# Optimization experiments

Hardware: AMD Instinct MI355X
Metric: run time of the kernel (lower is better)

The kernel has to match this reference:

```python
import jax, jax.numpy as jnp
import numpy as np

N_NODES = 262144
N_EDGES = 1048576
N_GRAPHS = 8192
IN_CH, HID, OUT_CH, N_LAYERS = 64, 256, 1, 3
SLOPE = 0.1  # LeakyReLU negative slope


def setup_inputs() -> dict:
    key = jax.random.key(0)
    ks = jax.random.split(key, 12)
    s = 0.05  # weight scale for numerical sanity
    return {
        "x": jax.random.normal(ks[0], (N_NODES, IN_CH), jnp.float32),
        "edge_index": jax.random.randint(ks[1], (2, N_EDGES), 0, N_NODES, jnp.int64),
        "batch": jnp.sort(jax.random.randint(ks[2], (N_NODES,), 0, N_GRAPHS, jnp.int64)),
        "embed_w": jax.random.normal(ks[3], (IN_CH, HID), jnp.float32) * s,
        "embed_b": jax.random.normal(ks[4], (HID,), jnp.float32) * s,
        "lin_l_w": jax.random.normal(ks[5], (N_LAYERS, HID, HID), jnp.float32) * s,
        "lin_l_b": jax.random.normal(ks[6], (N_LAYERS, HID), jnp.float32) * s,
        "lin_r_w": jax.random.normal(ks[7], (N_LAYERS, HID, HID), jnp.float32) * s,
        "lin1_w": jax.random.normal(ks[8], (HID, HID), jnp.float32) * s,
        "lin1_b": jax.random.normal(ks[9], (HID,), jnp.float32) * s,
        "lin2_w": jax.random.normal(ks[10], (HID, OUT_CH), jnp.float32) * s,
        "lin2_b": jax.random.normal(ks[11], (OUT_CH,), jnp.float32) * s,
    }


def reference(x, edge_index, batch, embed_w, embed_b, lin_l_w, lin_l_b, lin_r_w,
              lin1_w, lin1_b, lin2_w, lin2_b):
    n = x.shape[0]
    src, dst = edge_index[0], edge_index[1]  # messages flow src -> dst (PyG)
    # in-degree for mean aggregation, clamped to avoid div-by-zero
    deg = jax.ops.segment_sum(jnp.ones((src.shape[0],), x.dtype), dst, num_segments=n)
    inv_deg = (1.0 / jnp.maximum(deg, 1.0))[:, None]  # [N,1]

    h = x @ embed_w + embed_b  # [N, HID]
    for i in range(N_LAYERS):
        agg = jax.ops.segment_sum(h[src], dst, num_segments=n) * inv_deg  # mean over neighbors
        h = agg @ lin_l_w[i] + lin_l_b[i] + h @ lin_r_w[i]  # SAGEConv: lin_l(mean) + lin_r(x)
        if i < N_LAYERS - 1:
            h = jax.nn.leaky_relu(h, SLOPE)
    # global_add_pool over graphs in the batch
    pooled = jax.ops.segment_sum(h, batch, num_segments=N_GRAPHS)  # [G, HID]
    h = jax.nn.leaky_relu(pooled @ lin1_w + lin1_b, SLOPE)
    return h @ lin2_w + lin2_b  # [G, OUT_CH]
```

## Files before the change

kernel.cpp:

```cpp
#include <hip/hip_runtime.h>

typedef unsigned short u16;
typedef __bf16 bf16x8 __attribute__((ext_vector_type(8)));
typedef float f32x4 __attribute__((ext_vector_type(4)));
typedef unsigned short us8v __attribute__((ext_vector_type(8)));
typedef unsigned short us4v __attribute__((ext_vector_type(4)));

constexpr int NN = 262144;
constexpr int NE = 1048576;
constexpr int NG = 8192;
#define SLOPEF 0.1f

__device__ __forceinline__ float lrelu(float v) { return v > 0.f ? v : SLOPEF * v; }

__device__ __forceinline__ u16 f2bf(float f) {
  unsigned u = __builtin_bit_cast(unsigned, f);
  u += 0x7FFFu + ((u >> 16) & 1u);
  return (u16)(u >> 16);
}
__device__ __forceinline__ float bf2f(u16 s) {
  return __builtin_bit_cast(float, ((unsigned)s) << 16);
}

__device__ __align__(256) u16   g_HB[(size_t)NN * 256];
__device__ __align__(256) u16   g_AGG[(size_t)NN * 256];
__device__ __align__(256) u16   g_WTe[256 * 64];
__device__ __align__(256) u16   g_WTl[3 * 256 * 512];
__device__ __align__(256) int   g_indptr[NN + 1];
__device__ __align__(256) int   g_cursor[NN];
__device__ __align__(256) int   g_colsrc[NE];
__device__ __align__(256) int   g_bsum[256];
__device__ __align__(256) int   g_boff[256];
__device__ __align__(256) int   g_degi[NN];
__device__ __align__(256) float g_pooled[(size_t)NG * 256];

__global__ __launch_bounds__(256) void k_zero_deg() {
  g_degi[blockIdx.x * 256 + threadIdx.x] = 0;
}
__global__ __launch_bounds__(256) void k_zero_pool() {
  ((float4*)g_pooled)[blockIdx.x * 256 + threadIdx.x] = make_float4(0.f, 0.f, 0.f, 0.f);
}

__global__ __launch_bounds__(256) void k_convw(const float* __restrict__ embed_w,
    const float* __restrict__ lin_l_w, const float* __restrict__ lin_r_w) {
  int t = blockIdx.x * 256 + threadIdx.x;
  if (t < 16384) {
    int n = t >> 6, k = t & 63;
    g_WTe[t] = f2bf(embed_w[k * 256 + n]);
  } else {
    int u = t - 16384;
    int l = u >> 17;
    int r = u & 131071;
    int n = r >> 9, k = r & 511;
    float v = (k < 256) ? lin_l_w[(size_t)l * 65536 + k * 256 + n]
                        : lin_r_w[(size_t)l * 65536 + (k - 256) * 256 + n];
    g_WTl[(size_t)l * 131072 + n * 512 + k] = f2bf(v);
  }
}

__global__ __launch_bounds__(256) void k_deg(const int* __restrict__ dst) {
  int e = blockIdx.x * 256 + threadIdx.x;
  atomicAdd(&g_degi[dst[e]], 1);
}

__global__ __launch_bounds__(256) void k_scan1() {
  __shared__ int sm[256];
  int b = blockIdx.x, t = threadIdx.x;
  int4 v = *(const int4*)(g_degi + (size_t)b * 1024 + t * 4);
  int s = v.x + v.y + v.z + v.w;
  sm[t] = s; __syncthreads();
  for (int off = 1; off < 256; off <<= 1) {
    int x = (t >= off) ? sm[t - off] : 0; __syncthreads();
    sm[t] += x; __syncthreads();
  }
  if (t == 255) g_bsum[b] = sm[255];
}

__global__ __launch_bounds__(256) void k_scan2() {
  __shared__ int sm[256];
  int t = threadIdx.x;
  int v = g_bsum[t];
  sm[t] = v; __syncthreads();
  for (int off = 1; off < 256; off <<= 1) {
    int x = (t >= off) ? sm[t - off] : 0; __syncthreads();
    sm[t] += x; __syncthreads();
  }
  g_boff[t] = sm[t] - v;
  if (t == 255) g_indptr[NN] = sm[255];
}

__global__ __launch_bounds__(256) void k_scan3() {
  __shared__ int sm[256];
  int b = blockIdx.x, t = threadIdx.x;
  int4 v = *(const int4*)(g_degi + (size_t)b * 1024 + t * 4);
  int s = v.x + v.y + v.z + v.w;
  sm[t] = s; __syncthreads();
  for (int off = 1; off < 256; off <<= 1) {
    int x = (t >= off) ? sm[t - off] : 0; __syncthreads();
    sm[t] += x; __syncthreads();
  }
  int base = g_boff[b] + sm[t] - s;
  int i0 = b * 1024 + t * 4;
  g_indptr[i0]     = base;
  g_indptr[i0 + 1] = base + v.x;
  g_indptr[i0 + 2] = base + v.x + v.y;
  g_indptr[i0 + 3] = base + v.x + v.y + v.z;
}

__global__ __launch_bounds__(256) void k_invcur() {
  int n = blockIdx.x * 256 + threadIdx.x;
  float inv = 1.0f / fmaxf((float)g_degi[n], 1.0f);
  ((float*)g_degi)[n] = inv;
  g_cursor[n] = g_indptr[n];
}

__global__ __launch_bounds__(256) void k_fill(const int* __restrict__ ei) {
  int e = blockIdx.x * 256 + threadIdx.x;
  int src = ei[e], dst = ei[NE + e];
  int p = atomicAdd(&g_cursor[dst], 1);
  g_colsrc[p] = src;
}

__global__ __launch_bounds__(256) void k_gather() {
  int n = blockIdx.x * 4 + (threadIdx.x >> 6);
  int lane = threadIdx.x & 63;
  int s = g_indptr[n], e = g_indptr[n + 1];
  float a0 = 0.f, a1 = 0.f, a2 = 0.f, a3 = 0.f;
  for (int i = s; i < e; ++i) {
    int src = g_colsrc[i];
    us4v v = *(const us4v*)(g_HB + (size_t)src * 256 + lane * 4);
    a0 += bf2f(v[0]); a1 += bf2f(v[1]); a2 += bf2f(v[2]); a3 += bf2f(v[3]);
  }
  float w = ((const float*)g_degi)[n];
  us4v o;
  o[0] = f2bf(a0 * w); o[1] = f2bf(a1 * w); o[2] = f2bf(a2 * w); o[3] = f2bf(a3 * w);
  *(us4v*)(g_AGG + (size_t)n * 256 + lane * 4) = o;
}

template<int KSTEPS, int AMODE, bool LEAKY>
__global__ __launch_bounds__(256) void k_gemm(
    const float* __restrict__ Axf, const float* __restrict__ bias, int layer) {
  __shared__ __align__(16) unsigned char As[8192];
  __shared__ __align__(16) unsigned char Bs[32768];
  constexpr int LDW = AMODE ? 512 : 64;
  const u16* __restrict__ WT = AMODE ? (g_WTl + (size_t)layer * 131072) : g_WTe;
  const int tid = threadIdx.x;
  const int lane = tid & 63;
  const int w = tid >> 6;
  const int wr = w >> 1, wc = w & 1;
  const int m0 = blockIdx.x * 64;
  const int tg = tid & 7, tr = tid >> 3;

  f32x4 acc[2][8];
#pragma unroll
  for (int mi = 0; mi < 2; ++mi)
#pragma unroll
    for (int nj = 0; nj < 8; ++nj) acc[mi][nj] = (f32x4){0.f, 0.f, 0.f, 0.f};

  for (int s = 0; s < KSTEPS; ++s) {
    const int k0 = s * 64;
    us8v areg0, areg1;
    if (AMODE == 0) {
      const float* p0 = Axf + (size_t)(m0 + tr) * 64 + tg * 8;
      const float* p1 = Axf + (size_t)(m0 + tr + 32) * 64 + tg * 8;
      float4 f0 = *(const float4*)p0, f1 = *(const float4*)(p0 + 4);
      float4 g0 = *(const float4*)p1, g1 = *(const float4*)(p1 + 4);
      areg0[0] = f2bf(f0.x); areg0[1] = f2bf(f0.y); areg0[2] = f2bf(f0.z); areg0[3] = f2bf(f0.w);
      areg0[4] = f2bf(f1.x); areg0[5] = f2bf(f1.y); areg0[6] = f2bf(f1.z); areg0[7] = f2bf(f1.w);
      areg1[0] = f2bf(g0.x); areg1[1] = f2bf(g0.y); areg1[2] = f2bf(g0.z); areg1[3] = f2bf(g0.w);
      areg1[4] = f2bf(g1.x); areg1[5] = f2bf(g1.y); areg1[6] = f2bf(g1.z); areg1[7] = f2bf(g1.w);
    } else {
      const u16* src = (k0 < 256) ? (g_AGG + k0) : (g_HB + (k0 - 256));
      areg0 = *(const us8v*)(src + (size_t)(m0 + tr) * 256 + tg * 8);
      areg1 = *(const us8v*)(src + (size_t)(m0 + tr + 32) * 256 + tg * 8);
    }
    us8v breg[8];
#pragma unroll
    for (int it = 0; it < 8; ++it)
      breg[it] = *(const us8v*)(WT + (size_t)(tr + 32 * it) * LDW + k0 + tg * 8);
    __syncthreads();
    *(us8v*)(As + tg * 1024 + tr * 16) = areg0;
    *(us8v*)(As + tg * 1024 + (tr + 32) * 16) = areg1;
#pragma unroll
    for (int it = 0; it < 8; ++it)
      *(us8v*)(Bs + tg * 4096 + (tr + 32 * it) * 16) = breg[it];
    __syncthreads();
#pragma unroll
    for (int ks = 0; ks < 2; ++ks) {
      const int gsel = ks * 4 + (lane >> 4);
      bf16x8 a0 = *(const bf16x8*)(As + gsel * 1024 + (wr * 32 + (lane & 15)) * 16);
      bf16x8 a1 = *(const bf16x8*)(As + gsel * 1024 + (wr * 32 + 16 + (lane & 15)) * 16);
#pragma unroll
      for (int nj = 0; nj < 8; ++nj) {
        bf16x8 b = *(const bf16x8*)(Bs + gsel * 4096 + (wc * 128 + nj * 16 + (lane & 15)) * 16);
        acc[0][nj] = __builtin_amdgcn_mfma_f32_16x16x32_bf16(a0, b, acc[0][nj], 0, 0, 0);
        acc[1][nj] = __builtin_amdgcn_mfma_f32_16x16x32_bf16(a1, b, acc[1][nj], 0, 0, 0);
      }
    }
  }
#pragma unroll
  for (int mi = 0; mi < 2; ++mi)
#pragma unroll
    for (int nj = 0; nj < 8; ++nj) {
      const int col = wc * 128 + nj * 16 + (lane & 15);
      const float bb = bias[col];
#pragma unroll
      for (int j = 0; j < 4; ++j) {
        const int row = m0 + wr * 32 + mi * 16 + (lane >> 4) * 4 + j;
        float v = acc[mi][nj][j] + bb;
        if (LEAKY) v = lrelu(v);
        g_HB[(size_t)row * 256 + col] = f2bf(v);
      }
    }
}

__global__ __launch_bounds__(256) void k_pool(const int* __restrict__ batch) {
  int c = threadIdx.x;
  int n0 = blockIdx.x * 64;
  int gprev = batch[n0];
  float acc = 0.f;
  for (int i = 0; i < 64; ++i) {
    int n = n0 + i;
    int g = batch[n];
    if (g != gprev) {
      unsafeAtomicAdd(&g_pooled[(size_t)gprev * 256 + c], acc);
      acc = 0.f; gprev = g;
    }
    acc += bf2f(g_HB[(size_t)n * 256 + c]);
  }
  unsafeAtomicAdd(&g_pooled[(size_t)gprev * 256 + c], acc);
}

__global__ __launch_bounds__(256) void k_head(const float* __restrict__ w1,
    const float* __restrict__ b1, const float* __restrict__ w2, const float* __restrict__ b2,
    float* __restrict__ out) {
  __shared__ float p[256];
  __shared__ float red[256];
  int g = blockIdx.x, c = threadIdx.x;
  p[c] = g_pooled[(size_t)g * 256 + c];
  __syncthreads();
  float acc = b1[c];
#pragma unroll 8
  for (int k = 0; k < 256; ++k) acc = fmaf(p[k], w1[k * 256 + c], acc);
  acc = lrelu(acc) * w2[c];
  red[c] = acc;
  __syncthreads();
  for (int s = 128; s > 0; s >>= 1) {
    if (c < s) red[c] += red[c + s];
    __syncthreads();
  }
  if (c == 0) out[g] = red[0] + b2[0];
}

extern "C" void kernel_launch(void* const* d_in, const int* in_sizes, int n_in,
                              void* d_out, int out_size, void* d_ws, size_t ws_size,
                              hipStream_t stream) {
  const float* x       = (const float*)d_in[0];
  const int*   ei      = (const int*)d_in[1];
  const int*   batch   = (const int*)d_in[2];
  const float* embed_w = (const float*)d_in[3];
  const float* embed_b = (const float*)d_in[4];
  const float* lin_l_w = (const float*)d_in[5];
  const float* lin_l_b = (const float*)d_in[6];
  const float* lin_r_w = (const float*)d_in[7];
  const float* lin1_w  = (const float*)d_in[8];
  const float* lin1_b  = (const float*)d_in[9];
  const float* lin2_w  = (const float*)d_in[10];
  const float* lin2_b  = (const float*)d_in[11];
  float* out = (float*)d_out;
  (void)d_ws; (void)ws_size; (void)in_sizes; (void)n_in; (void)out_size;

  k_zero_deg <<<NN / 256, 256, 0, stream>>>();
  k_zero_pool<<<NG * 256 / (4 * 256), 256, 0, stream>>>();
  k_convw<<<(16384 + 3 * 131072) / 256, 256, 0, stream>>>(embed_w, lin_l_w, lin_r_w);
  k_deg  <<<NE / 256, 256, 0, stream>>>(ei + NE);
  k_scan1<<<256, 256, 0, stream>>>();
  k_scan2<<<1, 256, 0, stream>>>();
  k_scan3<<<256, 256, 0, stream>>>();
  k_invcur<<<NN / 256, 256, 0, stream>>>();
  k_fill <<<NE / 256, 256, 0, stream>>>(ei);

  k_gemm<1, 0, false><<<NN / 64, 256, 0, stream>>>(x, embed_b, 0);

  for (int i = 0; i < 3; ++i) {
    k_gather<<<NN / 4, 256, 0, stream>>>();
    const float* bb = lin_l_b + (size_t)i * 256;
    if (i < 2)
      k_gemm<8, 1, true><<<NN / 64, 256, 0, stream>>>(nullptr, bb, i);
    else
      k_gemm<8, 1, false><<<NN / 64, 256, 0, stream>>>(nullptr, bb, i);
  }

  k_pool<<<NN / 64, 256, 0, stream>>>(batch);
  k_head<<<NG, 256, 0, stream>>>(lin1_w, lin1_b, lin2_w, lin2_b, out);
}
```

Baseline: 1.444 ms.

## Enlarge GEMM row tile to 128 with swizzled LDS layout and unroll gather

The GEMM kernel now processes 128 rows per block instead of 64. Each wave computes a 64x128 output tile, which doubles reuse of the weight tile loaded into shared memory and halves the number of times weights are fetched from global memory. The shared memory layout changes to row-major with an XOR swizzle, meant to avoid bank conflicts on the fragment loads. The neighbor gather loop is unrolled by four so several source-row loads are in flight at once. The cost is more accumulator registers per thread and larger LDS use, which may lower occupancy.

```diff
diff --git a/kernel.cpp b/kernel.cpp
--- a/kernel.cpp
+++ b/kernel.cpp
@@ -126,7 +126,19 @@
   int lane = threadIdx.x & 63;
   int s = g_indptr[n], e = g_indptr[n + 1];
   float a0 = 0.f, a1 = 0.f, a2 = 0.f, a3 = 0.f;
-  for (int i = s; i < e; ++i) {
+  int i = s;
+  for (; i + 4 <= e; i += 4) {
+    int s0 = g_colsrc[i], s1 = g_colsrc[i + 1], s2 = g_colsrc[i + 2], s3 = g_colsrc[i + 3];
+    us4v v0 = *(const us4v*)(g_HB + (size_t)s0 * 256 + lane * 4);
+    us4v v1 = *(const us4v*)(g_HB + (size_t)s1 * 256 + lane * 4);
+    us4v v2 = *(const us4v*)(g_HB + (size_t)s2 * 256 + lane * 4);
+    us4v v3 = *(const us4v*)(g_HB + (size_t)s3 * 256 + lane * 4);
+    a0 += bf2f(v0[0]) + bf2f(v1[0]) + bf2f(v2[0]) + bf2f(v3[0]);
+    a1 += bf2f(v0[1]) + bf2f(v1[1]) + bf2f(v2[1]) + bf2f(v3[1]);
+    a2 += bf2f(v0[2]) + bf2f(v1[2]) + bf2f(v2[2]) + bf2f(v3[2]);
+    a3 += bf2f(v0[3]) + bf2f(v1[3]) + bf2f(v2[3]) + bf2f(v3[3]);
+  }
+  for (; i < e; ++i) {
     int src = g_colsrc[i];
     us4v v = *(const us4v*)(g_HB + (size_t)src * 256 + lane * 4);
     a0 += bf2f(v[0]); a1 += bf2f(v[1]); a2 += bf2f(v[2]); a3 += bf2f(v[3]);
@@ -140,7 +152,7 @@
 template<int KSTEPS, int AMODE, bool LEAKY>
 __global__ __launch_bounds__(256) void k_gemm(
     const float* __restrict__ Axf, const float* __restrict__ bias, int layer) {
-  __shared__ __align__(16) unsigned char As[8192];
+  __shared__ __align__(16) unsigned char As[16384];
   __shared__ __align__(16) unsigned char Bs[32768];
   constexpr int LDW = AMODE ? 512 : 64;
   const u16* __restrict__ WT = AMODE ? (g_WTl + (size_t)layer * 131072) : g_WTe;
@@ -148,65 +160,85 @@
   const int lane = tid & 63;
   const int w = tid >> 6;
   const int wr = w >> 1, wc = w & 1;
-  const int m0 = blockIdx.x * 64;
-  const int tg = tid & 7, tr = tid >> 3;
-
-  f32x4 acc[2][8];
-#pragma unroll
-  for (int mi = 0; mi < 2; ++mi)
+  const int m0 = blockIdx.x * 128;
+  const int srow = tid >> 1;
+  const int sj   = tid & 1;
+
+  f32x4 acc[4][8];
+#pragma unroll
+  for (int mi = 0; mi < 4; ++mi)
 #pragma unroll
     for (int nj = 0; nj < 8; ++nj) acc[mi][nj] = (f32x4){0.f, 0.f, 0.f, 0.f};
 
   for (int s = 0; s < KSTEPS; ++s) {
     const int k0 = s * 64;
-    us8v areg0, areg1;
+    us8v areg[4], breg[8];
     if (AMODE == 0) {
-      const float* p0 = Axf + (size_t)(m0 + tr) * 64 + tg * 8;
-      const float* p1 = Axf + (size_t)(m0 + tr + 32) * 64 + tg * 8;
-      float4 f0 = *(const float4*)p0, f1 = *(const float4*)(p0 + 4);
-      float4 g0 = *(const float4*)p1, g1 = *(const float4*)(p1 + 4);
-      areg0[0] = f2bf(f0.x); areg0[1] = f2bf(f0.y); areg0[2] = f2bf(f0.z); areg0[3] = f2bf(f0.w);
-      areg0[4] = f2bf(f1.x); areg0[5] = f2bf(f1.y); areg0[6] = f2bf(f1.z); areg0[7] = f2bf(f1.w);
-      areg1[0] = f2bf(g0.x); areg1[1] = f2bf(g0.y); areg1[2] = f2bf(g0.z); areg1[3] = f2bf(g0.w);
-      areg1[4] = f2bf(g1.x); areg1[5] = f2bf(g1.y); areg1[6] = f2bf(g1.z); areg1[7] = f2bf(g1.w);
+      const float* p = Axf + (size_t)(m0 + srow) * 64 + sj * 32;
+#pragma unroll
+      for (int i = 0; i < 4; ++i) {
+        float4 f0 = *(const float4*)(p + i * 8);
+        float4 f1 = *(const float4*)(p + i * 8 + 4);
+        areg[i][0] = f2bf(f0.x); areg[i][1] = f2bf(f0.y);
+        areg[i][2] = f2bf(f0.z); areg[i][3] = f2bf(f0.w);
+        areg[i][4] = f2bf(f1.x); areg[i][5] = f2bf(f1.y);
+        areg[i][6] = f2bf(f1.z); areg[i][7] = f2bf(f1.w);
+      }
     } else {
-      const u16* src = (k0 < 256) ? (g_AGG + k0) : (g_HB + (k0 - 256));
-      areg0 = *(const us8v*)(src + (size_t)(m0 + tr) * 256 + tg * 8);
-      areg1 = *(const us8v*)(src + (size_t)(m0 + tr + 32) * 256 + tg * 8);
-    }
-    us8v breg[8];
-#pragma unroll
-    for (int it = 0; it < 8; ++it)
-      breg[it] = *(const us8v*)(WT + (size_t)(tr + 32 * it) * LDW + k0 + tg * 8);
+      const u16* srcb = ((k0 < 256) ? (g_AGG + k0) : (g_HB + (k0 - 256)))
+                        + (size_t)(m0 + srow) * 256 + sj * 32;
+#pragma unroll
+      for (int i = 0; i < 4; ++i) areg[i] = *(const us8v*)(srcb + i * 8);
+    }
+#pragma unroll
+    for (int it = 0; it < 2; ++it) {
+      const int n = srow + it * 128;
+      const u16* srcb = WT + (size_t)n * LDW + k0 + sj * 32;
+#pragma unroll
+      for (int i = 0; i < 4; ++i) breg[it * 4 + i] = *(const us8v*)(srcb + i * 8);
+    }
     __syncthreads();
-    *(us8v*)(As + tg * 1024 + tr * 16) = areg0;
-    *(us8v*)(As + tg * 1024 + (tr + 32) * 16) = areg1;
-#pragma unroll
-    for (int it = 0; it < 8; ++it)
-      *(us8v*)(Bs + tg * 4096 + (tr + 32 * it) * 16) = breg[it];
+#pragma unroll
+    for (int i = 0; i < 4; ++i) {
+      const int g = sj * 4 + i;
+      *(us8v*)(As + srow * 128 + ((g ^ (srow & 7)) << 4)) = areg[i];
+    }
+#pragma unroll
+    for (int it = 0; it < 2; ++it) {
+      const int n = srow + it * 128;
+#pragma unroll
+      for (int i = 0; i < 4; ++i) {
+        const int g = sj * 4 + i;
+        *(us8v*)(Bs + n * 128 + ((g ^ (n & 7)) << 4)) = breg[it * 4 + i];
+      }
+    }
     __syncthreads();
 #pragma unroll
     for (int ks = 0; ks < 2; ++ks) {
       const int gsel = ks * 4 + (lane >> 4);
-      bf16x8 a0 = *(const bf16x8*)(As + gsel * 1024 + (wr * 32 + (lane & 15)) * 16);
-      bf16x8 a1 = *(const bf16x8*)(As + gsel * 1024 + (wr * 32 + 16 + (lane & 15)) * 16);
+      const int swz = (gsel ^ (lane & 7)) << 4;
+      bf16x8 a[4];
+#pragma unroll
+      for (int mi = 0; mi < 4; ++mi)
+        a[mi] = *(const bf16x8*)(As + (wr * 64 + mi * 16 + (lane & 15)) * 128 + swz);
 #pragma unroll
       for (int nj = 0; nj < 8; ++nj) {
-        bf16x8 b = *(const bf16x8*)(Bs + gsel * 4096 + (wc * 128 + nj * 16 + (lane & 15)) * 16);
-        acc[0][nj] = __builtin_amdgcn_mfma_f32_16x16x32_bf16(a0, b, acc[0][nj], 0, 0, 0);
-        acc[1][nj] = __builtin_amdgcn_mfma_f32_16x16x32_bf16(a1, b, acc[1][nj], 0, 0, 0);
+        bf16x8 b = *(const bf16x8*)(Bs + (wc * 128 + nj * 16 + (lane & 15)) * 128 + swz);
+#pragma unroll
+        for (int mi = 0; mi < 4; ++mi)
+          acc[mi][nj] = __builtin_amdgcn_mfma_f32_16x16x32_bf16(a[mi], b, acc[mi][nj], 0, 0, 0);
       }
     }
   }
 #pragma unroll
-  for (int mi = 0; mi < 2; ++mi)
+  for (int mi = 0; mi < 4; ++mi)
 #pragma unroll
     for (int nj = 0; nj < 8; ++nj) {
       const int col = wc * 128 + nj * 16 + (lane & 15);
       const float bb = bias[col];
 #pragma unroll
       for (int j = 0; j < 4; ++j) {
-        const int row = m0 + wr * 32 + mi * 16 + (lane >> 4) * 4 + j;
+        const int row = m0 + wr * 64 + mi * 16 + (lane >> 4) * 4 + j;
         float v = acc[mi][nj][j] + bb;
         if (LEAKY) v = lrelu(v);
         g_HB[(size_t)row * 256 + col] = f2bf(v);
@@ -280,15 +312,15 @@
   k_invcur<<<NN / 256, 256, 0, stream>>>();
   k_fill <<<NE / 256, 256, 0, stream>>>(ei);
 
-  k_gemm<1, 0, false><<<NN / 64, 256, 0, stream>>>(x, embed_b, 0);
+  k_gemm<1, 0, false><<<NN / 128, 256, 0, stream>>>(x, embed_b, 0);
 
   for (int i = 0; i < 3; ++i) {
     k_gather<<<NN / 4, 256, 0, stream>>>();
     const float* bb = lin_l_b + (size_t)i * 256;
     if (i < 2)
-      k_gemm<8, 1, true><<<NN / 64, 256, 0, stream>>>(nullptr, bb, i);
+      k_gemm<8, 1, true><<<NN / 128, 256, 0, stream>>>(nullptr, bb, i);
     else
-      k_gemm<8, 1, false><<<NN / 64, 256, 0, stream>>>(nullptr, bb, i);
+      k_gemm<8, 1, false><<<NN / 128, 256, 0, stream>>>(nullptr, bb, i);
   }
 
   k_pool<<<NN / 64, 256, 0, stream>>>(batch);
```

New measurement: 1.249 ms. 13.5% less time.
